# Optimization experiments

Hardware: AMD Instinct MI355X
Metric: run time of the kernel (lower is better)

Reference implementation:

```python
import jax, jax.numpy as jnp
import numpy as np
import math

EMBED_DIM = 128
NUM_HEADS = 8
HDIM = EMBED_DIM // NUM_HEADS


def setup_inputs() -> dict:
    key = jax.random.key(0)
    kq, kh, km, k1, k2, k3, k4 = jax.random.split(key, 7)
    B, NQ, GS = 32, 1024, 1024
    q = jax.random.normal(kq, (B, NQ, EMBED_DIM), dtype=jnp.float32)
    h = jax.random.normal(kh, (B, GS, EMBED_DIM), dtype=jnp.float32)
    mask = jax.random.bernoulli(km, 0.15, (B, NQ, GS))
    stdv = 1.0 / math.sqrt(HDIM)
    Wq = jax.random.uniform(k1, (NUM_HEADS, EMBED_DIM, HDIM), jnp.float32, -stdv, stdv)
    Wk = jax.random.uniform(k2, (NUM_HEADS, EMBED_DIM, HDIM), jnp.float32, -stdv, stdv)
    Wv = jax.random.uniform(k3, (NUM_HEADS, EMBED_DIM, HDIM), jnp.float32, -stdv, stdv)
    stdv_o = 1.0 / math.sqrt(EMBED_DIM)
    Wout = jax.random.uniform(k4, (NUM_HEADS, HDIM, EMBED_DIM), jnp.float32, -stdv_o, stdv_o)
    return {"q": q, "h": h, "mask": mask, "Wq": Wq, "Wk": Wk, "Wv": Wv, "Wout": Wout}


def reference(q, h, mask, Wq, Wk, Wv, Wout):
    norm = 1.0 / math.sqrt(HDIM)
    # per-head projections: [h, b, n, e]
    Q = jnp.einsum('bnd,hde->hbne', q, Wq)
    K = jnp.einsum('bgd,hde->hbge', h, Wk)
    V = jnp.einsum('bgd,hde->hbge', h, Wv)
    compat = norm * jnp.einsum('hbne,hbge->hbng', Q, K)  # [h,b,nq,gs]
    m = mask[None]  # broadcast over heads
    compat = jnp.where(m, -jnp.inf, compat)
    attn = jax.nn.softmax(compat, axis=-1)
    attn = jnp.where(m, 0.0, attn)
    heads = jnp.einsum('hbng,hbge->hbne', attn, V)
    out = jnp.einsum('hbne,hed->bnd', heads, Wout)
    return out
```

## Files before the change

### kernel.cpp

```cpp
#include <hip/hip_runtime.h>

typedef unsigned short u16;
typedef unsigned int   u32;
typedef short bf16x8 __attribute__((ext_vector_type(8)));
typedef float f32x4  __attribute__((ext_vector_type(4)));

#define NB  32
#define NQ  1024
#define GS  1024
#define NH  8
#define SCQ (0.25f * 1.4426950408889634f)
#define MBIG (-1.0e30f)

#define MFMA16(a, b, c) __builtin_amdgcn_mfma_f32_16x16x32_bf16(a, b, c, 0, 0, 0)

__device__ __forceinline__ u16 f2bf(float f) {
    u32 u = __float_as_uint(f);
    return (u16)((u + 0x7fffu + ((u >> 16) & 1u)) >> 16);
}
__device__ __forceinline__ u32 pk2bf(float a, float b) {
    u32 ua = __float_as_uint(a) + 0x8000u;
    u32 ub = __float_as_uint(b) + 0x8000u;
    return __builtin_amdgcn_perm(ub, ua, 0x07060302u);
}

__global__ __launch_bounds__(256) void wprep(const float* __restrict__ Wq,
                                             const float* __restrict__ Wk,
                                             const float* __restrict__ Wv,
                                             const float* __restrict__ Wout,
                                             u16* __restrict__ Wp) {
    int g = blockIdx.x * 256 + threadIdx.x;
    int m = g >> 14;
    int i = g & 16383;
    const float* src = (m == 0) ? Wq : (m == 1) ? Wk : (m == 2) ? Wv : Wout;
    float sc = (m == 0) ? SCQ : 1.0f;
    float v;
    if (m < 3) { int cc = i >> 7, k = i & 127;  v = src[(cc >> 4) * 2048 + k * 16 + (cc & 15)]; }
    else       { int d  = i >> 7, he = i & 127; v = src[(he >> 4) * 2048 + (he & 15) * 128 + d]; }
    Wp[m * 16384 + i] = f2bf(v * sc);
}

template <int MODE>
__device__ __forceinline__ void mgemm(const float* __restrict__ Ain,
                                      const u16* __restrict__ Wpm,
                                      u16* __restrict__ outb,
                                      u16* As, u16* Ws, int row0) {
    const int t    = threadIdx.x;
    const int wv   = t >> 6;
    const int lane = t & 63;
    const int quad = lane >> 4;
    const int c    = lane & 15;

#pragma unroll
    for (int g0 = 0; g0 < 2048; g0 += 256) {
        int g = g0 + t;
        int row = g >> 4, k0 = (g & 15) * 8;
        const float4* ap = (const float4*)&Ain[(size_t)(row0 + row) * 128 + k0];
        float4 a0 = ap[0], a1 = ap[1];
        int4 pk;
        pk.x = (int)pk2bf(a0.x, a0.y);
        pk.y = (int)pk2bf(a0.z, a0.w);
        pk.z = (int)pk2bf(a1.x, a1.y);
        pk.w = (int)pk2bf(a1.z, a1.w);
        *(int4*)&As[row * 136 + k0] = pk;
    }
#pragma unroll
    for (int g0 = 0; g0 < 2048; g0 += 256) {
        int g = g0 + t;
        int cc = g >> 4, k0 = (g & 15) * 8;
        *(int4*)&Ws[cc * 136 + k0] = *(const int4*)&Wpm[cc * 128 + k0];
    }
    __syncthreads();

    const f32x4 zf = {0.f, 0.f, 0.f, 0.f};
    f32x4 acc[2][8];
#pragma unroll
    for (int s = 0; s < 2; ++s)
#pragma unroll
        for (int j = 0; j < 8; ++j) acc[s][j] = zf;

#pragma unroll
    for (int kt = 0; kt < 4; ++kt) {
        bf16x8 af0 = *(const bf16x8*)&As[(wv * 32 + c) * 136 + kt * 32 + quad * 8];
        bf16x8 af1 = *(const bf16x8*)&As[(wv * 32 + 16 + c) * 136 + kt * 32 + quad * 8];
#pragma unroll
        for (int j = 0; j < 8; ++j) {
            bf16x8 bfr = *(const bf16x8*)&Ws[(j * 16 + c) * 136 + kt * 32 + quad * 8];
            acc[0][j] = MFMA16(af0, bfr, acc[0][j]);
            acc[1][j] = MFMA16(af1, bfr, acc[1][j]);
        }
    }

    __syncthreads();
    u16* Os = As;
#pragma unroll
    for (int s = 0; s < 2; ++s)
#pragma unroll
        for (int j = 0; j < 8; ++j)
#pragma unroll
            for (int r = 0; r < 4; ++r) {
                int lrow = wv * 32 + s * 16 + quad * 4 + r;
                int col  = j * 16 + c;
                u16 v = f2bf(acc[s][j][r]);
                if (MODE == 0) {
                    Os[lrow * 136 + col] = v;
                } else {
                    int tbp = (lrow & ~31) | (2 * (lrow & 15)) | ((lrow >> 4) & 1);
                    Os[col * 136 + tbp] = v;
                }
            }
    __syncthreads();

    if (MODE == 0) {
#pragma unroll
        for (int it = 0; it < 8; ++it) {
            int chunk = it * 256 + t;
            int lrow = chunk >> 4, c0 = (chunk & 15) * 8;
            *(int4*)&outb[(size_t)(row0 + lrow) * 128 + c0] =
                *(const int4*)&Os[lrow * 136 + c0];
        }
    } else {
        int bI = row0 >> 10, tb0 = row0 & 1023;
#pragma unroll
        for (int it = 0; it < 8; ++it) {
            int chunk = it * 256 + t;
            int col = chunk >> 4, t0 = (chunk & 15) * 8;
            *(int4*)&outb[(size_t)bI * (128 * 1024) + (size_t)col * 1024 + tb0 + t0] =
                *(const int4*)&Os[col * 136 + t0];
        }
    }
}

__global__ __launch_bounds__(256, 2) void proj_mfma(const float* __restrict__ q,
                                                    const float* __restrict__ h,
                                                    const u16* __restrict__ Wp,
                                                    u16* __restrict__ Qb,
                                                    u16* __restrict__ Kb,
                                                    u16* __restrict__ Vtg) {
    __shared__ u16 As[128 * 136];
    __shared__ u16 Ws[128 * 136];
    int row0 = blockIdx.x * 128;
    if (blockIdx.y == 0)      mgemm<0>(q, Wp,         Qb,  As, Ws, row0);
    else if (blockIdx.y == 1) mgemm<0>(h, Wp + 16384, Kb,  As, Ws, row0);
    else                      mgemm<2>(h, Wp + 32768, Vtg, As, Ws, row0);
}

__global__ __launch_bounds__(512, 4) void flash_mfma(const u16* __restrict__ Qb,
                                                     const u16* __restrict__ Kb,
                                                     const u16* __restrict__ Vtg,
                                                     const int* __restrict__ mask,
                                                     const u16* __restrict__ Wob,
                                                     float* __restrict__ out) {
    __shared__ u16 Kt[32 * 136];
    __shared__ u16 Vtt[128 * 36];
    __shared__ u16 Ps[NH][32 * 36];
    __shared__ float Mf[32 * 36];

    const int b    = blockIdx.x;
    const int q0   = blockIdx.y * 32;
    const int t    = threadIdx.x;
    const int hh   = t >> 6;
    const int lane = t & 63;
    const int quad = lane >> 4;
    const int c    = lane & 15;

    if (t < 128)
        *(u32*)&Kt[(t >> 2) * 136 + 128 + (t & 3) * 2] = 0u;

    const f32x4  zf = {0.f, 0.f, 0.f, 0.f};
    const bf16x8 zb = {0, 0, 0, 0, 0, 0, 0, 0};

    bf16x8 qf[2];
#pragma unroll
    for (int s = 0; s < 2; ++s) {
        qf[s] = zb;
        if (quad < 2)
            qf[s] = *(const bf16x8*)&Qb[((size_t)b * NQ + q0 + s * 16 + c) * 128 +
                                        hh * 16 + quad * 8];
    }

    f32x4 O[2] = {zf, zf};
    float ls[2][4] = {{0.f, 0.f, 0.f, 0.f}, {0.f, 0.f, 0.f, 0.f}};

    const int skey = t >> 4;
    const int sd0  = (t & 15) * 8;
    const int vdim = t >> 2;
    const int vs0  = (t & 3) * 8;
    const int mrow = t >> 4;
    const int mk0  = (t & 15) * 2;
    const int rp = (mrow & 3) | (((mrow >> 4) & 1) << 2) |
                   (((mrow >> 3) & 1) << 3) | (((mrow >> 2) & 1) << 4);

    const u16* Kptr = &Kb[((size_t)b * GS + skey) * 128 + sd0];
    const u16* Vptr = &Vtg[(size_t)b * (128 * 1024) + (size_t)vdim * 1024 + vs0];
    const int* Mptr = &mask[((size_t)b * NQ + q0 + mrow) * GS + mk0];

    int4 kreg = *(const int4*)Kptr;
    int4 vreg = *(const int4*)Vptr;
    int2 mreg = *(const int2*)Mptr;

    const int mfoff = ((quad >> 1) << 3) | ((quad & 1) << 4);

    for (int g0 = 0; g0 < GS; g0 += 32) {
        __syncthreads();
        *(int4*)&Kt[skey * 136 + sd0] = kreg;
        *(int4*)&Vtt[vdim * 36 + vs0] = vreg;
        Mf[mk0 * 36 + rp]       = mreg.x ? MBIG : 0.f;
        Mf[(mk0 + 1) * 36 + rp] = mreg.y ? MBIG : 0.f;
        __syncthreads();

        if (g0 + 32 < GS) {
            Kptr += 32 * 128;  kreg = *(const int4*)Kptr;
            Vptr += 32;        vreg = *(const int4*)Vptr;
            Mptr += 32;        mreg = *(const int2*)Mptr;
        }

        f32x4 sc[2][2];
#pragma unroll
        for (int kt = 0; kt < 2; ++kt) {
            bf16x8 kf = *(const bf16x8*)&Kt[(kt * 16 + c) * 136 + hh * 16 + quad * 8];
#pragma unroll
            for (int s = 0; s < 2; ++s) {
                f32x4 c0 = *(const f32x4*)&Mf[(kt * 16 + c) * 36 + (s << 2) + mfoff];
                sc[s][kt] = MFMA16(qf[s], kf, c0);
            }
        }
        bf16x8 vf = *(const bf16x8*)&Vtt[(hh * 16 + c) * 36 + quad * 8];

#pragma unroll
        for (int s = 0; s < 2; ++s) {
#pragma unroll
            for (int r = 0; r < 4; ++r) {
                float e0 = exp2f(sc[s][0][r]);
                float e1 = exp2f(sc[s][1][r]);
                ls[s][r] += e0 + e1;
                int row = s * 16 + quad * 4 + r;
                *(u32*)&Ps[hh][row * 36 + 2 * c] = pk2bf(e0, e1);
            }
        }

#pragma unroll
        for (int s = 0; s < 2; ++s) {
            bf16x8 pf = *(const bf16x8*)&Ps[hh][(s * 16 + c) * 36 + quad * 8];
            O[s] = MFMA16(pf, vf, O[s]);
        }
    }

    float rl[2][4];
#pragma unroll
    for (int s = 0; s < 2; ++s)
#pragma unroll
        for (int r = 0; r < 4; ++r) {
            float l = ls[s][r];
            l += __shfl_xor(l, 1);
            l += __shfl_xor(l, 2);
            l += __shfl_xor(l, 4);
            l += __shfl_xor(l, 8);
            rl[s][r] = (l > 0.f) ? 1.f / l : 0.f;
        }
    __syncthreads();
    u16* Hs = Kt;
#pragma unroll
    for (int s = 0; s < 2; ++s)
#pragma unroll
        for (int r = 0; r < 4; ++r)
            Hs[(s * 16 + quad * 4 + r) * 136 + hh * 16 + c] = f2bf(O[s][r] * rl[s][r]);
    __syncthreads();

    f32x4 oacc[2] = {zf, zf};
#pragma unroll
    for (int kt = 0; kt < 4; ++kt) {
        bf16x8 bfr = *(const bf16x8*)&Wob[(hh * 16 + c) * 128 + kt * 32 + quad * 8];
#pragma unroll
        for (int s = 0; s < 2; ++s) {
            bf16x8 af = *(const bf16x8*)&Hs[(s * 16 + c) * 136 + kt * 32 + quad * 8];
            oacc[s] = MFMA16(af, bfr, oacc[s]);
        }
    }
#pragma unroll
    for (int s = 0; s < 2; ++s)
#pragma unroll
        for (int r = 0; r < 4; ++r)
            out[((size_t)b * NQ + q0 + s * 16 + quad * 4 + r) * 128 + hh * 16 + c] =
                oacc[s][r];
}

extern "C" void kernel_launch(void* const* d_in, const int* in_sizes, int n_in,
                              void* d_out, int out_size, void* d_ws, size_t ws_size,
                              hipStream_t stream) {
    const float* q    = (const float*)d_in[0];
    const float* h    = (const float*)d_in[1];
    const int*   mask = (const int*)d_in[2];
    const float* Wq   = (const float*)d_in[3];
    const float* Wk   = (const float*)d_in[4];
    const float* Wv   = (const float*)d_in[5];
    const float* Wout = (const float*)d_in[6];
    float* out = (float*)d_out;

    const size_t NTOK = (size_t)NB * NQ;
    u16* Qb  = (u16*)d_ws;
    u16* Kb  = Qb + NTOK * 128;
    u16* Vtg = Kb + NTOK * 128;
    u16* Wp  = Vtg + NTOK * 128;

    wprep<<<dim3(256), 256, 0, stream>>>(Wq, Wk, Wv, Wout, Wp);
    proj_mfma<<<dim3(256, 3), 256, 0, stream>>>(q, h, Wp, Qb, Kb, Vtg);
    flash_mfma<<<dim3(NB, NQ / 32), 512, 0, stream>>>(Qb, Kb, Vtg, mask,
                                                      Wp + 49152, out);
}
```

Baseline: 312.6 us.

## Compute attention scores with one 32x32x16 MFMA per head and simplify softmax sums

The QK^T score step now uses a single 32x32x16 bf16 MFMA with K as the A operand and Q as B, producing a transposed 32-key by 32-query score tile. This replaces four 16x16x32 MFMAs that zero-padded half the reduction dimension. The mask tile and P tile layouts are simplified to row-major, with vector stores, and the row-sum reduction drops from four shuffles per value to one. The V-transpose permutation in the projection kernel is removed to match, and the launch-bounds occupancy hint rises from 4 to 8, which may force register spills.

```diff
diff --git a/kernel.cpp b/kernel.cpp
--- a/kernel.cpp
+++ b/kernel.cpp
@@ -3,7 +3,9 @@
 typedef unsigned short u16;
 typedef unsigned int   u32;
 typedef short bf16x8 __attribute__((ext_vector_type(8)));
+typedef float f32x2  __attribute__((ext_vector_type(2)));
 typedef float f32x4  __attribute__((ext_vector_type(4)));
+typedef float f32x16 __attribute__((ext_vector_type(16)));
 
 #define NB  32
 #define NQ  1024
@@ -13,6 +15,7 @@
 #define MBIG (-1.0e30f)
 
 #define MFMA16(a, b, c) __builtin_amdgcn_mfma_f32_16x16x32_bf16(a, b, c, 0, 0, 0)
+#define MFMA32(a, b, c) __builtin_amdgcn_mfma_f32_32x32x16_bf16(a, b, c, 0, 0, 0)
 
 __device__ __forceinline__ u16 f2bf(float f) {
     u32 u = __float_as_uint(f);
@@ -105,8 +108,7 @@
                 if (MODE == 0) {
                     Os[lrow * 136 + col] = v;
                 } else {
-                    int tbp = (lrow & ~31) | (2 * (lrow & 15)) | ((lrow >> 4) & 1);
-                    Os[col * 136 + tbp] = v;
+                    Os[col * 136 + lrow] = v;
                 }
             }
     __syncthreads();
@@ -145,7 +147,7 @@
     else                      mgemm<2>(h, Wp + 32768, Vtg, As, Ws, row0);
 }
 
-__global__ __launch_bounds__(512, 4) void flash_mfma(const u16* __restrict__ Qb,
+__global__ __launch_bounds__(512, 8) void flash_mfma(const u16* __restrict__ Qb,
                                                      const u16* __restrict__ Kb,
                                                      const u16* __restrict__ Vtg,
                                                      const int* __restrict__ mask,
@@ -163,24 +165,16 @@
     const int lane = t & 63;
     const int quad = lane >> 4;
     const int c    = lane & 15;
-
-    if (t < 128)
-        *(u32*)&Kt[(t >> 2) * 136 + 128 + (t & 3) * 2] = 0u;
-
-    const f32x4  zf = {0.f, 0.f, 0.f, 0.f};
-    const bf16x8 zb = {0, 0, 0, 0, 0, 0, 0, 0};
-
-    bf16x8 qf[2];
-#pragma unroll
-    for (int s = 0; s < 2; ++s) {
-        qf[s] = zb;
-        if (quad < 2)
-            qf[s] = *(const bf16x8*)&Qb[((size_t)b * NQ + q0 + s * 16 + c) * 128 +
-                                        hh * 16 + quad * 8];
-    }
+    const int qq   = lane & 31;
+    const int hi   = lane >> 5;
+
+    const f32x4 zf = {0.f, 0.f, 0.f, 0.f};
+
+    bf16x8 qf = *(const bf16x8*)&Qb[((size_t)b * NQ + q0 + qq) * 128 +
+                                    hh * 16 + hi * 8];
 
     f32x4 O[2] = {zf, zf};
-    float ls[2][4] = {{0.f, 0.f, 0.f, 0.f}, {0.f, 0.f, 0.f, 0.f}};
+    float lsum = 0.f;
 
     const int skey = t >> 4;
     const int sd0  = (t & 15) * 8;
@@ -188,8 +182,6 @@
     const int vs0  = (t & 3) * 8;
     const int mrow = t >> 4;
     const int mk0  = (t & 15) * 2;
-    const int rp = (mrow & 3) | (((mrow >> 4) & 1) << 2) |
-                   (((mrow >> 3) & 1) << 3) | (((mrow >> 2) & 1) << 4);
 
     const u16* Kptr = &Kb[((size_t)b * GS + skey) * 128 + sd0];
     const u16* Vptr = &Vtg[(size_t)b * (128 * 1024) + (size_t)vdim * 1024 + vs0];
@@ -198,15 +190,15 @@
     int4 kreg = *(const int4*)Kptr;
     int4 vreg = *(const int4*)Vptr;
     int2 mreg = *(const int2*)Mptr;
-
-    const int mfoff = ((quad >> 1) << 3) | ((quad & 1) << 4);
 
     for (int g0 = 0; g0 < GS; g0 += 32) {
         __syncthreads();
         *(int4*)&Kt[skey * 136 + sd0] = kreg;
         *(int4*)&Vtt[vdim * 36 + vs0] = vreg;
-        Mf[mk0 * 36 + rp]       = mreg.x ? MBIG : 0.f;
-        Mf[(mk0 + 1) * 36 + rp] = mreg.y ? MBIG : 0.f;
+        f32x2 mm;
+        mm.x = mreg.x ? MBIG : 0.f;
+        mm.y = mreg.y ? MBIG : 0.f;
+        *(f32x2*)&Mf[mrow * 36 + mk0] = mm;
         __syncthreads();
 
         if (g0 + 32 < GS) {
@@ -215,28 +207,31 @@
             Mptr += 32;        mreg = *(const int2*)Mptr;
         }
 
-        f32x4 sc[2][2];
-#pragma unroll
-        for (int kt = 0; kt < 2; ++kt) {
-            bf16x8 kf = *(const bf16x8*)&Kt[(kt * 16 + c) * 136 + hh * 16 + quad * 8];
-#pragma unroll
-            for (int s = 0; s < 2; ++s) {
-                f32x4 c0 = *(const f32x4*)&Mf[(kt * 16 + c) * 36 + (s << 2) + mfoff];
-                sc[s][kt] = MFMA16(qf[s], kf, c0);
-            }
-        }
+        bf16x8 kf = *(const bf16x8*)&Kt[qq * 136 + hh * 16 + hi * 8];
+        f32x16 c0;
+#pragma unroll
+        for (int blk = 0; blk < 4; ++blk) {
+            f32x4 m = *(const f32x4*)&Mf[qq * 36 + 8 * blk + 4 * hi];
+            c0[4 * blk + 0] = m.x;
+            c0[4 * blk + 1] = m.y;
+            c0[4 * blk + 2] = m.z;
+            c0[4 * blk + 3] = m.w;
+        }
+        f32x16 sc = MFMA32(kf, qf, c0);
+
         bf16x8 vf = *(const bf16x8*)&Vtt[(hh * 16 + c) * 36 + quad * 8];
 
-#pragma unroll
-        for (int s = 0; s < 2; ++s) {
-#pragma unroll
-            for (int r = 0; r < 4; ++r) {
-                float e0 = exp2f(sc[s][0][r]);
-                float e1 = exp2f(sc[s][1][r]);
-                ls[s][r] += e0 + e1;
-                int row = s * 16 + quad * 4 + r;
-                *(u32*)&Ps[hh][row * 36 + 2 * c] = pk2bf(e0, e1);
-            }
+        float e[16];
+#pragma unroll
+        for (int r = 0; r < 16; ++r) e[r] = __builtin_amdgcn_exp2f(sc[r]);
+        lsum += ((e[0] + e[1]) + (e[2] + e[3])) + ((e[4] + e[5]) + (e[6] + e[7])) +
+                (((e[8] + e[9]) + (e[10] + e[11])) + ((e[12] + e[13]) + (e[14] + e[15])));
+#pragma unroll
+        for (int blk = 0; blk < 4; ++blk) {
+            int2 pw;
+            pw.x = (int)pk2bf(e[4 * blk + 0], e[4 * blk + 1]);
+            pw.y = (int)pk2bf(e[4 * blk + 2], e[4 * blk + 3]);
+            *(int2*)&Ps[hh][qq * 36 + 8 * blk + 4 * hi] = pw;
         }
 
 #pragma unroll
@@ -246,25 +241,19 @@
         }
     }
 
-    float rl[2][4];
+    lsum += __shfl_xor(lsum, 32);
+    float rlv = (lsum > 0.f) ? 1.f / lsum : 0.f;
+
+    __syncthreads();
+    u16* Hs = Kt;
 #pragma unroll
     for (int s = 0; s < 2; ++s)
 #pragma unroll
         for (int r = 0; r < 4; ++r) {
-            float l = ls[s][r];
-            l += __shfl_xor(l, 1);
-            l += __shfl_xor(l, 2);
-            l += __shfl_xor(l, 4);
-            l += __shfl_xor(l, 8);
-            rl[s][r] = (l > 0.f) ? 1.f / l : 0.f;
-        }
-    __syncthreads();
-    u16* Hs = Kt;
-#pragma unroll
-    for (int s = 0; s < 2; ++s)
-#pragma unroll
-        for (int r = 0; r < 4; ++r)
-            Hs[(s * 16 + quad * 4 + r) * 136 + hh * 16 + c] = f2bf(O[s][r] * rl[s][r]);
+            float rlq = __shfl(rlv, s * 16 + quad * 4 + r);
+            Hs[(s * 16 + quad * 4 + r) * 136 + hh * 16 + c] =
+                f2bf(O[s][r] * rlq);
+        }
     __syncthreads();
 
     f32x4 oacc[2] = {zf, zf};
```

New measurement: 325.2 us. +4.0%, slower.
